# Optimization experiments

Measured on AMD Instinct MI355X. Metric: run time of the kernel, lower is better.

Reference implementation:

```python
import jax, jax.numpy as jnp
import numpy as np

N_NODES = 50000
N_EDGES = 400000
N_GRAPHS = 512
F = 32        # num_features
NB = 32       # mp_num_basis_fn
ZMAX = 118
CUTOFF = 5.0
NSPH = 9      # (mp_max_degree+1)^2 with max_degree=2
DEG_IDX = jnp.array([0, 1, 1, 1, 2, 2, 2, 2, 2])  # degree of each spherical component


def _bernstein(u, n=NB):
    # reciprocal_bernstein radial basis: Bernstein polynomials of degree n-1 at u in [0,1)
    k = jnp.arange(n, dtype=jnp.float32)
    log_binom = (jax.scipy.special.gammaln(float(n)) - jax.scipy.special.gammaln(k + 1.0)
                 - jax.scipy.special.gammaln(float(n) - k))
    u = jnp.clip(u, 1e-7, 1.0 - 1e-7)[..., None]
    return jnp.exp(log_binom + k * jnp.log(u) + (float(n) - 1.0 - k) * jnp.log1p(-u))


def _smooth_cutoff(r, cutoff=CUTOFF):
    t = r / cutoff
    return jnp.where(t < 1.0, jnp.exp(1.0 - 1.0 / jnp.clip(1.0 - t * t, 1e-7, None)), 0.0)


def _sph(u):
    # real spherical harmonics (cartesian normalization) up to degree 2; u: (E,3) unit vectors
    x, y, z = u[:, 0], u[:, 1], u[:, 2]
    c = jnp.sqrt(jnp.float32(3.0))
    return jnp.stack([jnp.ones_like(x), y, z, x,
                      c * x * y, c * y * z, 0.5 * (3.0 * z * z - 1.0),
                      c * z * x, 0.5 * c * (x * x - y * y)], axis=-1)


def _dense(x, W, b):
    # equivariant Dense: shared kernel over spherical components, bias only on scalar (l=0)
    y = jnp.einsum('nmf,fg->nmg', x, W)
    return y.at[:, 0, :].add(b)


def _silu_gate(x):
    # equivariant silu: scalar channel gates all degrees (scalar part -> exact silu)
    return x * jax.nn.sigmoid(x[:, 0:1, :])


def setup_inputs() -> dict:
    key = jax.random.key(0)
    ks = jax.random.split(key, 24)
    s = 1.0 / np.sqrt(F)
    sb = 1.0 / np.sqrt(NB)
    inp = {
        'positions': 2.0 * jax.random.normal(ks[0], (N_NODES, 3), jnp.float32),
        'embed': jax.random.normal(ks[1], (ZMAX, F), jnp.float32),
        'Wy0': sb * jax.random.normal(ks[2], (3, NB, F), jnp.float32),
        'Wx0': sb * jax.random.normal(ks[3], (3, NB, F), jnp.float32),
        'W1_0': s * jax.random.normal(ks[4], (F, F), jnp.float32),
        'b1_0': jnp.zeros((F,), jnp.float32),
        'W2_0': s * jax.random.normal(ks[5], (F, F), jnp.float32),
        'b2_0': jnp.zeros((F,), jnp.float32),
        'c0': jnp.full((1,), 0.5, jnp.float32),
        'Wr_last': sb * jax.random.normal(ks[6], (NB, F), jnp.float32),
        'W1_1': s * jax.random.normal(ks[7], (F, F), jnp.float32),
        'b1_1': jnp.zeros((F,), jnp.float32),
        'W2_1': s * jax.random.normal(ks[8], (F, F), jnp.float32),
        'b2_1': jnp.zeros((F,), jnp.float32),
        'c1': jnp.full((1,), 0.5, jnp.float32),
        'Wro1': s * jax.random.normal(ks[9], (F, F), jnp.float32),
        'bro1': jnp.zeros((F,), jnp.float32),
        'Wro2': s * jax.random.normal(ks[10], (F, 1), jnp.float32),
        'bro2': jnp.zeros((1,), jnp.float32),
        'atomic_bias': jax.random.normal(ks[11], (ZMAX,), jnp.float32),
        'atomic_numbers': jax.random.randint(ks[12], (N_NODES,), 0, ZMAX, jnp.int32),
        'dst_idx': jax.random.randint(ks[13], (N_EDGES,), 0, N_NODES, jnp.int32),
        'src_idx': jax.random.randint(ks[14], (N_EDGES,), 0, N_NODES, jnp.int32),
        'batch_segments': jnp.sort(jax.random.randint(ks[15], (N_NODES,), 0, N_GRAPHS, jnp.int32)),
        'graph_mask': jnp.ones((N_GRAPHS,), jnp.bool_),
    }
    return inp


def reference(positions, embed, Wy0, Wx0, W1_0, b1_0, W2_0, b2_0, c0,
              Wr_last, W1_1, b1_1, W2_1, b2_1, c1,
              Wro1, bro1, Wro2, bro2, atomic_bias,
              atomic_numbers, dst_idx, src_idx, batch_segments, graph_mask):
    # --- edge geometry (gather_src/gather_dst) ---
    disp = positions[src_idx] - positions[dst_idx]                # (E,3)
    r = jnp.sqrt(jnp.sum(disp * disp, axis=-1) + 1e-12)           # (E,)
    u = disp / r[:, None]
    Y = _sph(u)                                                   # (E,9)
    rbf = _bernstein(r / (r + 1.0)) * _smooth_cutoff(r)[:, None]  # (E,NB)

    # --- atomic embedding, lifted to (N, 9, F) with zero higher degrees ---
    x0 = embed[atomic_numbers]                                    # (N,F)
    x = jnp.concatenate([x0[:, None, :], jnp.zeros((N_NODES, NSPH - 1, F), x0.dtype)], axis=1)

    # --- iteration 0: full-degree equivariant message pass ---
    wy = jnp.einsum('eb,lbf->elf', rbf, Wy0)[:, DEG_IDX, :]       # (E,9,F) radial weights, (0,l)->l path
    wx = jnp.einsum('eb,lbf->elf', rbf, Wx0)[:, DEG_IDX, :]       # (l,0)->l path
    xs = x[src_idx]                                               # (E,9,F)
    msg = wy * Y[:, :, None] * xs[:, 0:1, :] + wx * xs
    y = jax.ops.segment_sum(msg, dst_idx, num_segments=N_NODES)   # (N,9,F)
    y = x + y
    y = _silu_gate(_dense(y, W1_0, b1_0))
    y = _dense(y, W2_0, b2_0)
    x = x + jax.nn.silu(c0) * y                                   # y_nl == 0 (era disabled)

    # --- iteration 1 (last): max_degree=0 message pass, then reduce to scalars ---
    w0 = rbf @ Wr_last                                            # (E,F)
    msg0 = w0 * x[src_idx, 0, :]
    y0 = jax.ops.segment_sum(msg0, dst_idx, num_segments=N_NODES) # (N,F)
    xs0 = x[:, 0, :]                                              # change_max_degree -> scalars
    y0 = xs0 + y0
    y0 = jax.nn.silu(y0 @ W1_1 + b1_1)
    y0 = y0 @ W2_1 + b2_1
    xs0 = xs0 + jax.nn.silu(c1) * y0

    # --- atomic readout and per-graph sum ---
    h = jax.nn.silu(xs0 @ Wro1 + bro1)
    e_atom = (h @ Wro2)[:, 0] + bro2[0] + atomic_bias[atomic_numbers]
    e_graph = jax.ops.segment_sum(e_atom, batch_segments, num_segments=N_GRAPHS)
    return jnp.where(graph_mask, e_graph, 0.0)
```

## Files before the change

kernel.cpp:

```cpp
#include <hip/hip_runtime.h>
#include <math.h>

#define NNODES 50000
#define NEDGES 400000
#define NGRAPHS 512
#define FDIM 32
#define CAP 64

static constexpr float BINOM31[32] = {
    1.f, 31.f, 465.f, 4495.f, 31465.f, 169911.f, 736281.f, 2629575.f,
    7888725.f, 20160075.f, 44352165.f, 84672315.f, 141120525.f, 206253075.f,
    265182525.f, 300540195.f, 300540195.f, 265182525.f, 206253075.f,
    141120525.f, 84672315.f, 44352165.f, 20160075.f, 7888725.f, 2629575.f,
    736281.f, 169911.f, 31465.f, 4495.f, 465.f, 31.f, 1.f
};

__device__ __forceinline__ float fast_rcp(float x) {
    return __builtin_amdgcn_rcpf(x);
}
__device__ __forceinline__ float silu(float x) {
    return x * fast_rcp(1.0f + __expf(-x));
}

__global__ __launch_bounds__(256) void prep(
    const float* __restrict__ pos, float4* __restrict__ pos4,
    int* __restrict__ deg, float* __restrict__ out)
{
    int i = blockIdx.x * 256 + threadIdx.x;
    if (i < NGRAPHS) out[i] = 0.0f;
    if (i < NNODES) {
        pos4[i] = make_float4(pos[3 * i], pos[3 * i + 1], pos[3 * i + 2], 0.f);
        deg[i] = 0;
    }
}

__global__ __launch_bounds__(256) void build_csr(
    const float4* __restrict__ pos4,
    const int* __restrict__ srci, const int* __restrict__ dsti,
    const int* __restrict__ Z,
    float4* __restrict__ pay, int* __restrict__ deg)
{
    int e = blockIdx.x * 256 + threadIdx.x;
    if (e >= NEDGES) return;
    int s = srci[e], d = dsti[e];
    float4 ps = pos4[s];
    float4 pd = pos4[d];
    float dx = ps.x - pd.x, dy = ps.y - pd.y, dz = ps.z - pd.z;
    float r = sqrtf(dx * dx + dy * dy + dz * dz + 1e-12f);
    if (r >= 5.0f) return;

    float t = r * 0.2f;
    float q = fmaxf(1.0f - t * t, 1e-7f);
    float cut = __expf(1.0f - fast_rcp(q));
    float v = fast_rcp(r + 1.0f);
    float v2 = v * v, v4 = v2 * v2, v8 = v4 * v4, v16 = v8 * v8;
    float scale = v16 * v8 * v4 * v2 * v * cut;

    int rank = atomicAdd(&deg[d], 1);
    if (rank < CAP)
        pay[(size_t)d * CAP + rank] =
            make_float4(r, scale, __int_as_float(s), __int_as_float(Z[s]));
}

#define DECLC(K) float C##K; { float _w = Wp1[K * FDIM + f];               \
                               if (Wp2) _w += Wp2[K * FDIM + f];           \
                               C##K = BINOM31[K] * _w; }
#define DECL_ALL_C                                                          \
    DECLC(0)  DECLC(1)  DECLC(2)  DECLC(3)  DECLC(4)  DECLC(5)  DECLC(6)   \
    DECLC(7)  DECLC(8)  DECLC(9)  DECLC(10) DECLC(11) DECLC(12) DECLC(13)  \
    DECLC(14) DECLC(15) DECLC(16) DECLC(17) DECLC(18) DECLC(19) DECLC(20)  \
    DECLC(21) DECLC(22) DECLC(23) DECLC(24) DECLC(25) DECLC(26) DECLC(27)  \
    DECLC(28) DECLC(29) DECLC(30) DECLC(31)

#define HEO(KE, KO)                                                        \
    _ea = fmaf(_ea, _r2a, C##KE); _oa = fmaf(_oa, _r2a, C##KO);            \
    _eb = fmaf(_eb, _r2b, C##KE); _ob = fmaf(_ob, _r2b, C##KO);            \
    _ec = fmaf(_ec, _r2c, C##KE); _oc = fmaf(_oc, _r2c, C##KO);            \
    _ed = fmaf(_ed, _r2d, C##KE); _od = fmaf(_od, _r2d, C##KO);

#define GATHER_ACC4(XSRC, ROWSEL)                                          \
    float accv = 0.0f;                                                     \
    for (int j = 0; j < dg; j += 4) {                                      \
        int _j1 = min(j + 1, dg - 1);                                      \
        int _j2 = min(j + 2, dg - 1);                                      \
        int _j3 = min(j + 3, dg - 1);                                      \
        float4 _pa = slot[j];   float4 _pb = slot[_j1];                    \
        float4 _pc = slot[_j2]; float4 _pd = slot[_j3];                    \
        float _sa = _pa.y;                                                 \
        float _sb = (j + 1 < dg) ? _pb.y : 0.f;                            \
        float _sc = (j + 2 < dg) ? _pc.y : 0.f;                            \
        float _sd = (j + 3 < dg) ? _pd.y : 0.f;                            \
        float _xa = (XSRC)[(size_t)__float_as_int(_pa.ROWSEL) * FDIM + f]; \
        float _xb = (XSRC)[(size_t)__float_as_int(_pb.ROWSEL) * FDIM + f]; \
        float _xc = (XSRC)[(size_t)__float_as_int(_pc.ROWSEL) * FDIM + f]; \
        float _xd = (XSRC)[(size_t)__float_as_int(_pd.ROWSEL) * FDIM + f]; \
        float _r2a = _pa.x * _pa.x, _r2b = _pb.x * _pb.x;                  \
        float _r2c = _pc.x * _pc.x, _r2d = _pd.x * _pd.x;                  \
        float _ea = C30, _oa = C31, _eb = C30, _ob = C31;                  \
        float _ec = C30, _oc = C31, _ed = C30, _od = C31;                  \
        HEO(28, 29) HEO(26, 27) HEO(24, 25) HEO(22, 23) HEO(20, 21)       \
        HEO(18, 19) HEO(16, 17) HEO(14, 15) HEO(12, 13) HEO(10, 11)       \
        HEO(8, 9)   HEO(6, 7)   HEO(4, 5)   HEO(2, 3)   HEO(0, 1)         \
        float _wa = fmaf(_pa.x, _oa, _ea);                                 \
        float _wb = fmaf(_pb.x, _ob, _eb);                                 \
        float _wc = fmaf(_pc.x, _oc, _ec);                                 \
        float _wd = fmaf(_pd.x, _od, _ed);                                 \
        accv = fmaf(_sa * _wa, _xa, accv);                                 \
        accv = fmaf(_sb * _wb, _xb, accv);                                 \
        accv = fmaf(_sc * _wc, _xc, accv);                                 \
        accv = fmaf(_sd * _wd, _xd, accv);                                 \
    }

#define MATVEC32L(RES, WL, YP, BIAS) do {                                  \
    float4 _q0=(YP)[0], _q1=(YP)[1], _q2=(YP)[2], _q3=(YP)[3];             \
    float4 _q4=(YP)[4], _q5=(YP)[5], _q6=(YP)[6], _q7=(YP)[7];             \
    float _a0=(BIAS), _a1=0.f, _a2=0.f, _a3=0.f;                           \
    _a0=fmaf(_q0.x,(WL)[ 0*FDIM+f],_a0); _a0=fmaf(_q0.y,(WL)[ 1*FDIM+f],_a0); \
    _a0=fmaf(_q0.z,(WL)[ 2*FDIM+f],_a0); _a0=fmaf(_q0.w,(WL)[ 3*FDIM+f],_a0); \
    _a1=fmaf(_q1.x,(WL)[ 4*FDIM+f],_a1); _a1=fmaf(_q1.y,(WL)[ 5*FDIM+f],_a1); \
    _a1=fmaf(_q1.z,(WL)[ 6*FDIM+f],_a1); _a1=fmaf(_q1.w,(WL)[ 7*FDIM+f],_a1); \
    _a2=fmaf(_q2.x,(WL)[ 8*FDIM+f],_a2); _a2=fmaf(_q2.y,(WL)[ 9*FDIM+f],_a2); \
    _a2=fmaf(_q2.z,(WL)[10*FDIM+f],_a2); _a2=fmaf(_q2.w,(WL)[11*FDIM+f],_a2); \
    _a3=fmaf(_q3.x,(WL)[12*FDIM+f],_a3); _a3=fmaf(_q3.y,(WL)[13*FDIM+f],_a3); \
    _a3=fmaf(_q3.z,(WL)[14*FDIM+f],_a3); _a3=fmaf(_q3.w,(WL)[15*FDIM+f],_a3); \
    _a0=fmaf(_q4.x,(WL)[16*FDIM+f],_a0); _a0=fmaf(_q4.y,(WL)[17*FDIM+f],_a0); \
    _a0=fmaf(_q4.z,(WL)[18*FDIM+f],_a0); _a0=fmaf(_q4.w,(WL)[19*FDIM+f],_a0); \
    _a1=fmaf(_q5.x,(WL)[20*FDIM+f],_a1); _a1=fmaf(_q5.y,(WL)[21*FDIM+f],_a1); \
    _a1=fmaf(_q5.z,(WL)[22*FDIM+f],_a1); _a1=fmaf(_q5.w,(WL)[23*FDIM+f],_a1); \
    _a2=fmaf(_q6.x,(WL)[24*FDIM+f],_a2); _a2=fmaf(_q6.y,(WL)[25*FDIM+f],_a2); \
    _a2=fmaf(_q6.z,(WL)[26*FDIM+f],_a2); _a2=fmaf(_q6.w,(WL)[27*FDIM+f],_a2); \
    _a3=fmaf(_q7.x,(WL)[28*FDIM+f],_a3); _a3=fmaf(_q7.y,(WL)[29*FDIM+f],_a3); \
    _a3=fmaf(_q7.z,(WL)[30*FDIM+f],_a3); _a3=fmaf(_q7.w,(WL)[31*FDIM+f],_a3); \
    RES = (_a0+_a1)+(_a2+_a3); } while (0)

__global__ __launch_bounds__(256, 4) void fused_a(
    const float4* __restrict__ pay, const int* __restrict__ deg,
    const float* __restrict__ embed, const int* __restrict__ Z,
    const float* __restrict__ Wy0, const float* __restrict__ Wx0,
    const float* __restrict__ W1, const float* __restrict__ b1,
    const float* __restrict__ W2, const float* __restrict__ b2,
    const float* __restrict__ c0,
    float* __restrict__ x1buf)
{
    __shared__ __align__(16) float ylds[4][64];
    __shared__ float W1l[FDIM * FDIM];
    __shared__ float W2l[FDIM * FDIM];
    int tid = threadIdx.x;
    for (int i = tid; i < FDIM * FDIM; i += 256) {
        W1l[i] = W1[i];
        W2l[i] = W2[i];
    }
    __syncthreads();

    int widx = tid >> 6;
    int lane = tid & 63;
    int f    = lane & 31;
    int half = lane >> 5;

    const float* Wp1 = Wy0;
    const float* Wp2 = Wx0;
    DECL_ALL_C

    int n = (blockIdx.x * 4 + widx) * 2 + half;
    const float4* slot = pay + (size_t)n * CAP;
    int dg = min(deg[n], CAP);

    GATHER_ACC4(embed, w)

    float x0 = embed[Z[n] * FDIM + f];
    float yv = x0 + accv;

    float* yrow = &ylds[widx][half * 32];
    const float4* yp = (const float4*)yrow;
    yrow[f] = yv;
    float t;
    MATVEC32L(t, W1l, yp, b1[f]);
    t = silu(t);
    yrow[f] = t;
    float u;
    MATVEC32L(u, W2l, yp, b2[f]);
    x1buf[(size_t)n * FDIM + f] = fmaf(silu(c0[0]), u, x0);
}

__global__ __launch_bounds__(256, 4) void fused_b(
    const float4* __restrict__ pay, const int* __restrict__ deg,
    const float* __restrict__ x1buf, const float* __restrict__ Wr_last,
    const float* __restrict__ W1, const float* __restrict__ b1,
    const float* __restrict__ W2, const float* __restrict__ b2,
    const float* __restrict__ c1,
    const float* __restrict__ Wro1, const float* __restrict__ bro1,
    const float* __restrict__ Wro2, const float* __restrict__ bro2,
    const float* __restrict__ abias, const int* __restrict__ Z,
    const int* __restrict__ segs,
    float* __restrict__ out)
{
    __shared__ __align__(16) float ylds[4][64];
    __shared__ float W1l[FDIM * FDIM];
    __shared__ float W2l[FDIM * FDIM];
    __shared__ float Wrl[FDIM * FDIM];
    __shared__ float eb[8];
    __shared__ int   sb[8];
    int tid = threadIdx.x;
    for (int i = tid; i < FDIM * FDIM; i += 256) {
        W1l[i] = W1[i];
        W2l[i] = W2[i];
        Wrl[i] = Wro1[i];
    }
    __syncthreads();

    int widx = tid >> 6;
    int lane = tid & 63;
    int f    = lane & 31;
    int half = lane >> 5;

    const float* Wp1 = Wr_last;
    const float* Wp2 = nullptr;
    DECL_ALL_C

    int n = (blockIdx.x * 4 + widx) * 2 + half;
    const float4* slot = pay + (size_t)n * CAP;
    int dg = min(deg[n], CAP);

    GATHER_ACC4(x1buf, z)

    float x1 = x1buf[(size_t)n * FDIM + f];
    float yv = x1 + accv;

    float* yrow = &ylds[widx][half * 32];
    const float4* yp = (const float4*)yrow;
    yrow[f] = yv;
    float t;
    MATVEC32L(t, W1l, yp, b1[f]);
    t = silu(t);
    yrow[f] = t;
    float u;
    MATVEC32L(u, W2l, yp, b2[f]);
    float xs0 = fmaf(silu(c1[0]), u, x1);
    yrow[f] = xs0;
    float h;
    MATVEC32L(h, Wrl, yp, bro1[f]);
    float p = silu(h) * Wro2[f];
    p += __shfl_xor(p, 16, 32);
    p += __shfl_xor(p, 8, 32);
    p += __shfl_xor(p, 4, 32);
    p += __shfl_xor(p, 2, 32);
    p += __shfl_xor(p, 1, 32);

    if (f == 0) {
        eb[widx * 2 + half] = p + bro2[0] + abias[Z[n]];
        sb[widx * 2 + half] = segs[n];
    }
    __syncthreads();
    if (tid == 0) {
        float acc = eb[0];
        int cur = sb[0];
        #pragma unroll
        for (int i = 1; i < 8; ++i) {
            if (sb[i] == cur) acc += eb[i];
            else { atomicAdd(&out[cur], acc); cur = sb[i]; acc = eb[i]; }
        }
        atomicAdd(&out[cur], acc);
    }
}

extern "C" void kernel_launch(void* const* d_in, const int* in_sizes, int n_in,
                              void* d_out, int out_size, void* d_ws, size_t ws_size,
                              hipStream_t stream)
{
    const float* pos     = (const float*)d_in[0];
    const float* embed   = (const float*)d_in[1];
    const float* Wy0     = (const float*)d_in[2];
    const float* Wx0     = (const float*)d_in[3];
    const float* W1_0    = (const float*)d_in[4];
    const float* b1_0    = (const float*)d_in[5];
    const float* W2_0    = (const float*)d_in[6];
    const float* b2_0    = (const float*)d_in[7];
    const float* c0      = (const float*)d_in[8];
    const float* Wr_last = (const float*)d_in[9];
    const float* W1_1    = (const float*)d_in[10];
    const float* b1_1    = (const float*)d_in[11];
    const float* W2_1    = (const float*)d_in[12];
    const float* b2_1    = (const float*)d_in[13];
    const float* c1      = (const float*)d_in[14];
    const float* Wro1    = (const float*)d_in[15];
    const float* bro1    = (const float*)d_in[16];
    const float* Wro2    = (const float*)d_in[17];
    const float* bro2    = (const float*)d_in[18];
    const float* abias   = (const float*)d_in[19];
    const int*   Z       = (const int*)d_in[20];
    const int*   dsti    = (const int*)d_in[21];
    const int*   srci    = (const int*)d_in[22];
    const int*   segs    = (const int*)d_in[23];

    float* out = (float*)d_out;

    char* w = (char*)d_ws;
    float4* pay   = (float4*)w;  w += (size_t)NNODES * CAP * 16;
    float*  x1buf = (float*)w;   w += (size_t)NNODES * FDIM * 4;
    float4* pos4  = (float4*)w;  w += (size_t)NNODES * 16;
    int*    deg   = (int*)w;     w += (size_t)NNODES * 4;

    const int edgeBlocks = (NEDGES + 255) / 256;
    const int nodeBlocks = NNODES / 8;
    const int prepBlocks = (NNODES + 255) / 256;

    prep<<<prepBlocks, 256, 0, stream>>>(pos, pos4, deg, out);
    build_csr<<<edgeBlocks, 256, 0, stream>>>(pos4, srci, dsti, Z, pay, deg);
    fused_a<<<nodeBlocks, 256, 0, stream>>>(pay, deg, embed, Z, Wy0, Wx0,
                                            W1_0, b1_0, W2_0, b2_0, c0, x1buf);
    fused_b<<<nodeBlocks, 256, 0, stream>>>(pay, deg, x1buf, Wr_last,
                                            W1_1, b1_1, W2_1, b2_1, c1,
                                            Wro1, bro1, Wro2, bro2,
                                            abias, Z, segs, out);
}
```

Before: 204.7 us.

## Process two nodes per half-wave, precompute Bernstein weights, shrink edge slot capacity

The binomial-scaled radial weights are now computed once in the prep kernel instead of being rebuilt in every thread of both fused kernels. Each half-wave now handles two nodes, so block setup, LDS weight staging and the 32 coefficient register loads are shared across twice as many nodes, and half as many blocks are launched. The per-node edge slot capacity drops from 64 to 32, which shrinks and densifies the payload buffer. The cost is that any node with more than 32 in-cutoff incoming edges would silently lose messages, and the extra serial work per thread reduces parallelism.

```diff
diff --git a/kernel.cpp b/kernel.cpp
--- a/kernel.cpp
+++ b/kernel.cpp
@@ -5,7 +5,7 @@
 #define NEDGES 400000
 #define NGRAPHS 512
 #define FDIM 32
-#define CAP 64
+#define CAP 32
 
 static constexpr float BINOM31[32] = {
     1.f, 31.f, 465.f, 4495.f, 31465.f, 169911.f, 736281.f, 2629575.f,
@@ -23,11 +23,20 @@
 }
 
 __global__ __launch_bounds__(256) void prep(
-    const float* __restrict__ pos, float4* __restrict__ pos4,
-    int* __restrict__ deg, float* __restrict__ out)
+    const float* __restrict__ pos,
+    const float* __restrict__ Wy0, const float* __restrict__ Wx0,
+    const float* __restrict__ Wr_last,
+    float4* __restrict__ pos4, int* __restrict__ deg,
+    float* __restrict__ out,
+    float* __restrict__ cwA, float* __restrict__ cwB)
 {
     int i = blockIdx.x * 256 + threadIdx.x;
     if (i < NGRAPHS) out[i] = 0.0f;
+    if (i < FDIM * FDIM) {
+        float b = BINOM31[i >> 5];
+        cwA[i] = b * (Wy0[i] + Wx0[i]);
+        cwB[i] = b * Wr_last[i];
+    }
     if (i < NNODES) {
         pos4[i] = make_float4(pos[3 * i], pos[3 * i + 1], pos[3 * i + 2], 0.f);
         deg[i] = 0;
@@ -62,15 +71,15 @@
             make_float4(r, scale, __int_as_float(s), __int_as_float(Z[s]));
 }
 
-#define DECLC(K) float C##K; { float _w = Wp1[K * FDIM + f];               \
-                               if (Wp2) _w += Wp2[K * FDIM + f];           \
-                               C##K = BINOM31[K] * _w; }
-#define DECL_ALL_C                                                          \
-    DECLC(0)  DECLC(1)  DECLC(2)  DECLC(3)  DECLC(4)  DECLC(5)  DECLC(6)   \
-    DECLC(7)  DECLC(8)  DECLC(9)  DECLC(10) DECLC(11) DECLC(12) DECLC(13)  \
-    DECLC(14) DECLC(15) DECLC(16) DECLC(17) DECLC(18) DECLC(19) DECLC(20)  \
-    DECLC(21) DECLC(22) DECLC(23) DECLC(24) DECLC(25) DECLC(26) DECLC(27)  \
-    DECLC(28) DECLC(29) DECLC(30) DECLC(31)
+#define DECLC(CW, K) float C##K = (CW)[(K) * FDIM + f];
+#define DECL_ALL_C(CW)                                                      \
+    DECLC(CW,0)  DECLC(CW,1)  DECLC(CW,2)  DECLC(CW,3)  DECLC(CW,4)        \
+    DECLC(CW,5)  DECLC(CW,6)  DECLC(CW,7)  DECLC(CW,8)  DECLC(CW,9)        \
+    DECLC(CW,10) DECLC(CW,11) DECLC(CW,12) DECLC(CW,13) DECLC(CW,14)       \
+    DECLC(CW,15) DECLC(CW,16) DECLC(CW,17) DECLC(CW,18) DECLC(CW,19)       \
+    DECLC(CW,20) DECLC(CW,21) DECLC(CW,22) DECLC(CW,23) DECLC(CW,24)       \
+    DECLC(CW,25) DECLC(CW,26) DECLC(CW,27) DECLC(CW,28) DECLC(CW,29)       \
+    DECLC(CW,30) DECLC(CW,31)
 
 #define HEO(KE, KO)                                                        \
     _ea = fmaf(_ea, _r2a, C##KE); _oa = fmaf(_oa, _r2a, C##KO);            \
@@ -78,18 +87,19 @@
     _ec = fmaf(_ec, _r2c, C##KE); _oc = fmaf(_oc, _r2c, C##KO);            \
     _ed = fmaf(_ed, _r2d, C##KE); _od = fmaf(_od, _r2d, C##KO);
 
-#define GATHER_ACC4(XSRC, ROWSEL)                                          \
-    float accv = 0.0f;                                                     \
-    for (int j = 0; j < dg; j += 4) {                                      \
-        int _j1 = min(j + 1, dg - 1);                                      \
-        int _j2 = min(j + 2, dg - 1);                                      \
-        int _j3 = min(j + 3, dg - 1);                                      \
-        float4 _pa = slot[j];   float4 _pb = slot[_j1];                    \
-        float4 _pc = slot[_j2]; float4 _pd = slot[_j3];                    \
+#define GATHER_ACC4(ACC, XSRC, ROWSEL, SLOT, DG)                           \
+    float ACC = 0.0f;                                                      \
+    for (int j = 0; j < (DG); j += 4) {                                    \
+        int _jm = (DG) - 1;                                                \
+        int _j1 = min(j + 1, _jm);                                         \
+        int _j2 = min(j + 2, _jm);                                         \
+        int _j3 = min(j + 3, _jm);                                         \
+        float4 _pa = (SLOT)[j];    float4 _pb = (SLOT)[_j1];               \
+        float4 _pc = (SLOT)[_j2];  float4 _pd = (SLOT)[_j3];               \
         float _sa = _pa.y;                                                 \
-        float _sb = (j + 1 < dg) ? _pb.y : 0.f;                            \
-        float _sc = (j + 2 < dg) ? _pc.y : 0.f;                            \
-        float _sd = (j + 3 < dg) ? _pd.y : 0.f;                            \
+        float _sb = (j + 1 < (DG)) ? _pb.y : 0.f;                          \
+        float _sc = (j + 2 < (DG)) ? _pc.y : 0.f;                          \
+        float _sd = (j + 3 < (DG)) ? _pd.y : 0.f;                          \
         float _xa = (XSRC)[(size_t)__float_as_int(_pa.ROWSEL) * FDIM + f]; \
         float _xb = (XSRC)[(size_t)__float_as_int(_pb.ROWSEL) * FDIM + f]; \
         float _xc = (XSRC)[(size_t)__float_as_int(_pc.ROWSEL) * FDIM + f]; \
@@ -105,10 +115,10 @@
         float _wb = fmaf(_pb.x, _ob, _eb);                                 \
         float _wc = fmaf(_pc.x, _oc, _ec);                                 \
         float _wd = fmaf(_pd.x, _od, _ed);                                 \
-        accv = fmaf(_sa * _wa, _xa, accv);                                 \
-        accv = fmaf(_sb * _wb, _xb, accv);                                 \
-        accv = fmaf(_sc * _wc, _xc, accv);                                 \
-        accv = fmaf(_sd * _wd, _xd, accv);                                 \
+        ACC = fmaf(_sa * _wa, _xa, ACC);                                   \
+        ACC = fmaf(_sb * _wb, _xb, ACC);                                   \
+        ACC = fmaf(_sc * _wc, _xc, ACC);                                   \
+        ACC = fmaf(_sd * _wd, _xd, ACC);                                   \
     }
 
 #define MATVEC32L(RES, WL, YP, BIAS) do {                                  \
@@ -133,10 +143,27 @@
     _a3=fmaf(_q7.z,(WL)[30*FDIM+f],_a3); _a3=fmaf(_q7.w,(WL)[31*FDIM+f],_a3); \
     RES = (_a0+_a1)+(_a2+_a3); } while (0)
 
+#define PROC_A(NN)                                                         \
+    {                                                                      \
+        const float4* slot = pay + (size_t)(NN) * CAP;                     \
+        int dg = min(deg[NN], CAP);                                        \
+        GATHER_ACC4(accv, embed, w, slot, dg)                              \
+        float x0 = embed[Z[NN] * FDIM + f];                                \
+        float yv = x0 + accv;                                              \
+        yrow[f] = yv;                             \
+        float t;                                                           \
+        MATVEC32L(t, W1l, yp, b1f);                                        \
+        t = silu(t);                                  \
+        yrow[f] = t;                                                       \
+        float u;                                                           \
+        MATVEC32L(u, W2l, yp, b2f);                                        \
+        x1buf[(size_t)(NN) * FDIM + f] = fmaf(sc0, u, x0);                 \
+    }
+
 __global__ __launch_bounds__(256, 4) void fused_a(
     const float4* __restrict__ pay, const int* __restrict__ deg,
     const float* __restrict__ embed, const int* __restrict__ Z,
-    const float* __restrict__ Wy0, const float* __restrict__ Wx0,
+    const float* __restrict__ cwA,
     const float* __restrict__ W1, const float* __restrict__ b1,
     const float* __restrict__ W2, const float* __restrict__ b2,
     const float* __restrict__ c0,
@@ -157,34 +184,51 @@
     int f    = lane & 31;
     int half = lane >> 5;
 
-    const float* Wp1 = Wy0;
-    const float* Wp2 = Wx0;
-    DECL_ALL_C
-
-    int n = (blockIdx.x * 4 + widx) * 2 + half;
-    const float4* slot = pay + (size_t)n * CAP;
-    int dg = min(deg[n], CAP);
-
-    GATHER_ACC4(embed, w)
-
-    float x0 = embed[Z[n] * FDIM + f];
-    float yv = x0 + accv;
+    DECL_ALL_C(cwA)
+    float b1f = b1[f], b2f = b2[f];
+    float sc0 = silu(c0[0]);
 
     float* yrow = &ylds[widx][half * 32];
     const float4* yp = (const float4*)yrow;
-    yrow[f] = yv;
-    float t;
-    MATVEC32L(t, W1l, yp, b1[f]);
-    t = silu(t);
-    yrow[f] = t;
-    float u;
-    MATVEC32L(u, W2l, yp, b2[f]);
-    x1buf[(size_t)n * FDIM + f] = fmaf(silu(c0[0]), u, x0);
-}
+
+    int base = blockIdx.x * 16 + (widx * 2 + half) * 2;
+    PROC_A(base)
+    PROC_A(base + 1)
+}
+
+#define PROC_B(NN, EIDX)                                                   \
+    {                                                                      \
+        const float4* slot = pay + (size_t)(NN) * CAP;                     \
+        int dg = min(deg[NN], CAP);                                        \
+        GATHER_ACC4(accv, x1buf, z, slot, dg)                              \
+        float x1 = x1buf[(size_t)(NN) * FDIM + f];                         \
+        float yv = x1 + accv;                                              \
+        yrow[f] = yv;                                                      \
+        float t;                                                           \
+        MATVEC32L(t, W1l, yp, b1f);                                        \
+        t = silu(t);                                                       \
+        yrow[f] = t;                                                       \
+        float u;                                                           \
+        MATVEC32L(u, W2l, yp, b2f);                                        \
+        float xs0 = fmaf(sc1, u, x1);                                      \
+        yrow[f] = xs0;                                                     \
+        float h;                                                           \
+        MATVEC32L(h, Wrl, yp, brf);                                        \
+        float p = silu(h) * w2f;                                           \
+        p += __shfl_xor(p, 16, 32);                                        \
+        p += __shfl_xor(p, 8, 32);                                         \
+        p += __shfl_xor(p, 4, 32);                                         \
+        p += __shfl_xor(p, 2, 32);                                         \
+        p += __shfl_xor(p, 1, 32);                                         \
+        if (f == 0) {                                                      \
+            eb[EIDX] = p + br2 + abias[Z[NN]];                             \
+            sb[EIDX] = segs[NN];                                           \
+        }                                                                  \
+    }
 
 __global__ __launch_bounds__(256, 4) void fused_b(
     const float4* __restrict__ pay, const int* __restrict__ deg,
-    const float* __restrict__ x1buf, const float* __restrict__ Wr_last,
+    const float* __restrict__ x1buf, const float* __restrict__ cwB,
     const float* __restrict__ W1, const float* __restrict__ b1,
     const float* __restrict__ W2, const float* __restrict__ b2,
     const float* __restrict__ c1,
@@ -198,8 +242,8 @@
     __shared__ float W1l[FDIM * FDIM];
     __shared__ float W2l[FDIM * FDIM];
     __shared__ float Wrl[FDIM * FDIM];
-    __shared__ float eb[8];
-    __shared__ int   sb[8];
+    __shared__ float eb[16];
+    __shared__ int   sb[16];
     int tid = threadIdx.x;
     for (int i = tid; i < FDIM * FDIM; i += 256) {
         W1l[i] = W1[i];
@@ -213,49 +257,25 @@
     int f    = lane & 31;
     int half = lane >> 5;
 
-    const float* Wp1 = Wr_last;
-    const float* Wp2 = nullptr;
-    DECL_ALL_C
-
-    int n = (blockIdx.x * 4 + widx) * 2 + half;
-    const float4* slot = pay + (size_t)n * CAP;
-    int dg = min(deg[n], CAP);
-
-    GATHER_ACC4(x1buf, z)
-
-    float x1 = x1buf[(size_t)n * FDIM + f];
-    float yv = x1 + accv;
+    DECL_ALL_C(cwB)
+    float b1f = b1[f], b2f = b2[f], brf = bro1[f], w2f = Wro2[f];
+    float sc1 = silu(c1[0]);
+    float br2 = bro2[0];
 
     float* yrow = &ylds[widx][half * 32];
     const float4* yp = (const float4*)yrow;
-    yrow[f] = yv;
-    float t;
-    MATVEC32L(t, W1l, yp, b1[f]);
-    t = silu(t);
-    yrow[f] = t;
-    float u;
-    MATVEC32L(u, W2l, yp, b2[f]);
-    float xs0 = fmaf(silu(c1[0]), u, x1);
-    yrow[f] = xs0;
-    float h;
-    MATVEC32L(h, Wrl, yp, bro1[f]);
-    float p = silu(h) * Wro2[f];
-    p += __shfl_xor(p, 16, 32);
-    p += __shfl_xor(p, 8, 32);
-    p += __shfl_xor(p, 4, 32);
-    p += __shfl_xor(p, 2, 32);
-    p += __shfl_xor(p, 1, 32);
-
-    if (f == 0) {
-        eb[widx * 2 + half] = p + bro2[0] + abias[Z[n]];
-        sb[widx * 2 + half] = segs[n];
-    }
+
+    int hidx = widx * 2 + half;
+    int base = blockIdx.x * 16 + hidx * 2;
+    PROC_B(base,     hidx * 2)
+    PROC_B(base + 1, hidx * 2 + 1)
+
     __syncthreads();
     if (tid == 0) {
         float acc = eb[0];
         int cur = sb[0];
         #pragma unroll
-        for (int i = 1; i < 8; ++i) {
+        for (int i = 1; i < 16; ++i) {
             if (sb[i] == cur) acc += eb[i];
             else { atomicAdd(&out[cur], acc); cur = sb[i]; acc = eb[i]; }
         }
@@ -299,16 +319,19 @@
     float*  x1buf = (float*)w;   w += (size_t)NNODES * FDIM * 4;
     float4* pos4  = (float4*)w;  w += (size_t)NNODES * 16;
     int*    deg   = (int*)w;     w += (size_t)NNODES * 4;
+    float*  cwA   = (float*)w;   w += FDIM * FDIM * 4;
+    float*  cwB   = (float*)w;   w += FDIM * FDIM * 4;
 
     const int edgeBlocks = (NEDGES + 255) / 256;
-    const int nodeBlocks = NNODES / 8;
+    const int nodeBlocks = NNODES / 16;
     const int prepBlocks = (NNODES + 255) / 256;
 
-    prep<<<prepBlocks, 256, 0, stream>>>(pos, pos4, deg, out);
+    prep<<<prepBlocks, 256, 0, stream>>>(pos, Wy0, Wx0, Wr_last,
+                                         pos4, deg, out, cwA, cwB);
     build_csr<<<edgeBlocks, 256, 0, stream>>>(pos4, srci, dsti, Z, pay, deg);
-    fused_a<<<nodeBlocks, 256, 0, stream>>>(pay, deg, embed, Z, Wy0, Wx0,
+    fused_a<<<nodeBlocks, 256, 0, stream>>>(pay, deg, embed, Z, cwA,
                                             W1_0, b1_0, W2_0, b2_0, c0, x1buf);
-    fused_b<<<nodeBlocks, 256, 0, stream>>>(pay, deg, x1buf, Wr_last,
+    fused_b<<<nodeBlocks, 256, 0, stream>>>(pay, deg, x1buf, cwB,
                                             W1_1, b1_1, W2_1, b2_1, c1,
                                             Wro1, bro1, Wro2, bro2,
                                             abias, Z, segs, out);
```

New measurement: 239.5 us. 17.0% more time.
